# Kernel tuning notes

Measured on AMD Instinct MI355X. Metric: run time of the kernel, lower is better.

Reference implementation:

```python
import jax, jax.numpy as jnp
import numpy as np

EPS = 1e-15


def setup_inputs() -> dict:
    key = jax.random.key(0)
    k1, k2, k3 = jax.random.split(key, 3)
    B, F, C, T = 8, 257, 8, 3000
    X_real = jax.random.normal(k1, (B, F, C, T), dtype=jnp.float32)
    X_imag = jax.random.normal(k2, (B, F, C, T), dtype=jnp.float32)
    mask = jax.random.uniform(k3, (B, F, T), dtype=jnp.float32)
    return {"X_real": X_real, "X_imag": X_imag, "mask": mask}


def reference(X_real, X_imag, mask):
    # X: (B, F, C, T) complex STFT
    X = X_real + 1j * X_imag
    # normalize mask over time (normalize=True)
    m = mask / (jnp.sum(mask, axis=-1, keepdims=True) + EPS)  # (B,F,T)
    # Fused masked time-weighted outer product: equivalent to
    # einsum('...ct,...et->...tce') * mask then sum over t, but contracts
    # t directly (batched GEMM) without the (B,F,T,C,C) intermediate.
    Xm = X * m[..., None, :]                                  # (B,F,C,T)
    psd = jnp.einsum('bfct,bfet->bfce', Xm, jnp.conj(X))      # (B,F,C,C)
    return psd
```

## Files before the change

kernel.cpp:

```cpp
#include <hip/hip_runtime.h>

#define T_LEN 3000
#define TQ2 1500
#define C_CH 8
#define NTHREADS 256
#define NWAVES 4


#define XPOSE_ROUND(OFF)                                        \
    {                                                           \
        const bool hi = (lane & (OFF)) != 0;                    \
        _Pragma("unroll")                                       \
        for (int i = 0; i < (OFF); ++i) {                       \
            float send = hi ? acc[i] : acc[i + (OFF)];          \
            float recv = __shfl_xor(send, (OFF));               \
            float keep = hi ? acc[i + (OFF)] : acc[i];          \
            acc[i] = keep + recv;                               \
        }                                                       \
    }

__global__ __launch_bounds__(NTHREADS) void psd_kernel(
        const float* __restrict__ Xr,
        const float* __restrict__ Xi,
        const float* __restrict__ Mk,
        float* __restrict__ out,
        int real_elems, int write_imag) {
    const int slice = blockIdx.x;
    const int tid   = threadIdx.x;
    const int lane  = tid & 63;
    const int wave  = tid >> 6;

    const float2* xr2 = reinterpret_cast<const float2*>(Xr) + (size_t)slice * (C_CH * TQ2);
    const float2* xi2 = reinterpret_cast<const float2*>(Xi) + (size_t)slice * (C_CH * TQ2);
    const float2* mk2 = reinterpret_cast<const float2*>(Mk) + (size_t)slice * TQ2;

    float acc[64];
#pragma unroll
    for (int k = 0; k < 64; ++k) acc[k] = 0.f;
    float s = 0.f;

    for (int q = tid; q < TQ2; q += NTHREADS) {
        float2 mv = mk2[q];
        s += mv.x + mv.y;
        float ar[C_CH][2], ai[C_CH][2];
#pragma unroll
        for (int c = 0; c < C_CH; ++c) {
            float2 v = xr2[c * TQ2 + q];
            ar[c][0] = v.x; ar[c][1] = v.y;
            float2 w = xi2[c * TQ2 + q];
            ai[c][0] = w.x; ai[c][1] = w.y;
        }
        const float mm[2] = {mv.x, mv.y};
#pragma unroll
        for (int j = 0; j < 2; ++j) {
            const float m = mm[j];
            float mr[C_CH], mi[C_CH];
#pragma unroll
            for (int c = 0; c < C_CH; ++c) {
                mr[c] = m * ar[c][j];
                mi[c] = m * ai[c][j];
            }
#pragma unroll
            for (int c = 0; c < C_CH; ++c)
                acc[c] += mr[c] * ar[c][j] + mi[c] * ai[c][j];
#pragma unroll
            for (int c = 0; c < C_CH; ++c) {
#pragma unroll
                for (int e = c + 1; e < C_CH; ++e) {
                    const int p = 7 * c - (c * (c - 1)) / 2 + (e - c - 1);
                    acc[8 + p]  += mr[c] * ar[e][j] + mi[c] * ai[e][j];
                    acc[36 + p] += mi[c] * ar[e][j] - mr[c] * ai[e][j];
                }
            }
        }
    }

#pragma unroll
    for (int off = 32; off > 0; off >>= 1) s += __shfl_xor(s, off);

    XPOSE_ROUND(32)
    XPOSE_ROUND(16)
    XPOSE_ROUND(8)
    XPOSE_ROUND(4)
    XPOSE_ROUND(2)
    XPOSE_ROUND(1)

    __shared__ float red[NWAVES * 64];
    __shared__ float sred[NWAVES];
    __shared__ float fin[128];
    red[wave * 64 + lane] = acc[0];
    if (lane == 0) sred[wave] = s;
    __syncthreads();

    if (tid < 64) {
        float tot = (red[tid] + red[64 + tid]) + (red[128 + tid] + red[192 + tid]);
        const float stot = (sred[0] + sred[1]) + (sred[2] + sred[3]);
        tot *= 1.0f / (stot + 1e-15f);

        if (tid < 8) {
            const int c = tid;
            fin[c * 8 + c]      = tot;
            fin[64 + c * 8 + c] = 0.f;
        } else {
            int p = (tid < 36) ? (tid - 8) : (tid - 36);
            int c = 0;
            while (p >= 7 - c) { p -= 7 - c; ++c; }
            const int e = c + 1 + p;
            if (tid < 36) {
                fin[c * 8 + e] = tot;
                fin[e * 8 + c] = tot;
            } else {
                fin[64 + c * 8 + e] = tot;
                fin[64 + e * 8 + c] = -tot;
            }
        }
    }
    __syncthreads();
    if (tid < 64) {
        out[(size_t)slice * 64 + tid] = fin[tid];
    } else if (tid < 128 && write_imag) {
        out[(size_t)real_elems + (size_t)slice * 64 + (tid - 64)] = fin[tid];
    }
}

extern "C" void kernel_launch(void* const* d_in, const int* in_sizes, int n_in,
                              void* d_out, int out_size, void* d_ws, size_t ws_size,
                              hipStream_t stream) {
    const float* Xr = (const float*)d_in[0];
    const float* Xi = (const float*)d_in[1];
    const float* Mk = (const float*)d_in[2];
    float* out = (float*)d_out;
    const int slices = in_sizes[2] / T_LEN;
    const int real_elems = slices * 64;
    const int write_imag = (out_size >= 2 * real_elems) ? 1 : 0;
    psd_kernel<<<dim3(slices), dim3(NTHREADS), 0, stream>>>(Xr, Xi, Mk, out,
                                                            real_elems, write_imag);
}
```

Measured before the change: 404.1 us.

## Double-buffer time chunks into LDS with async global_load_lds prefetch

New measurement: 410.6 us. About the same (+1.6%).

```diff
diff --git a/kernel.cpp b/kernel.cpp
--- a/kernel.cpp
+++ b/kernel.cpp
@@ -1,11 +1,17 @@
 #include <hip/hip_runtime.h>
 
 #define T_LEN 3000
-#define TQ2 1500
 #define C_CH 8
 #define NTHREADS 256
 #define NWAVES 4
+#define TT 256
+#define NCHUNK 12
+#define NSTREAM 17
 
+#define AS1 __attribute__((address_space(1)))
+#define AS3 __attribute__((address_space(3)))
+#define GLOAD_LDS(G, L) \
+    __builtin_amdgcn_global_load_lds((const AS1 void*)(G), (AS3 void*)(L), 16, 0, 0)
 
 #define XPOSE_ROUND(OFF)                                        \
     {                                                           \
@@ -19,7 +25,29 @@
         }                                                       \
     }
 
-__global__ __launch_bounds__(NTHREADS) void psd_kernel(
+__device__ __forceinline__ void stage(const float* __restrict__ Xr,
+                                      const float* __restrict__ Xi,
+                                      const float* __restrict__ Mk,
+                                      float* buf, int slice, int off,
+                                      int wave, int lane) {
+    int elem = off + lane * 4;
+    if (elem > T_LEN - 4) elem = T_LEN - 4;
+    const size_t xbase = (size_t)slice * (C_CH * T_LEN);
+#pragma unroll
+    for (int k = 0; k < 4; ++k) {
+        const int s = wave + 4 * k;
+        const float* g = (s < 8)
+            ? (Xr + xbase + (size_t)s * T_LEN + elem)
+            : (Xi + xbase + (size_t)(s - 8) * T_LEN + elem);
+        GLOAD_LDS(g, buf + s * TT);
+    }
+    if (wave == 0) {
+        const float* g = Mk + (size_t)slice * T_LEN + elem;
+        GLOAD_LDS(g, buf + 16 * TT);
+    }
+}
+
+__global__ __launch_bounds__(NTHREADS, 4) void psd_kernel(
         const float* __restrict__ Xr,
         const float* __restrict__ Xi,
         const float* __restrict__ Mk,
@@ -30,49 +58,62 @@
     const int lane  = tid & 63;
     const int wave  = tid >> 6;
 
-    const float2* xr2 = reinterpret_cast<const float2*>(Xr) + (size_t)slice * (C_CH * TQ2);
-    const float2* xi2 = reinterpret_cast<const float2*>(Xi) + (size_t)slice * (C_CH * TQ2);
-    const float2* mk2 = reinterpret_cast<const float2*>(Mk) + (size_t)slice * TQ2;
+    __shared__ float lds[2][NSTREAM * TT];
+    __shared__ float red[NWAVES * 64];
+    __shared__ float sred[NWAVES];
+    __shared__ float fin[128];
 
     float acc[64];
 #pragma unroll
     for (int k = 0; k < 64; ++k) acc[k] = 0.f;
     float s = 0.f;
 
-    for (int q = tid; q < TQ2; q += NTHREADS) {
-        float2 mv = mk2[q];
-        s += mv.x + mv.y;
-        float ar[C_CH][2], ai[C_CH][2];
+    stage(Xr, Xi, Mk, lds[0], slice, 0, wave, lane);
+
+    for (int ch = 0; ch < NCHUNK; ++ch) {
+        const int cur = ch & 1;
+        if (ch + 1 < NCHUNK) {
+            stage(Xr, Xi, Mk, lds[cur ^ 1], slice, (ch + 1) * TT, wave, lane);
+            if (wave == 0) asm volatile("s_waitcnt vmcnt(5)" ::: "memory");
+            else           asm volatile("s_waitcnt vmcnt(4)" ::: "memory");
+        } else {
+            asm volatile("s_waitcnt vmcnt(0)" ::: "memory");
+        }
+        __builtin_amdgcn_s_barrier();
+
+        const int rem   = T_LEN - ch * TT;
+        const int valid = rem < TT ? rem : TT;
+        const float* buf = lds[cur];
+        if (tid < valid) {
+            const float m = buf[16 * TT + tid];
+            s += m;
+            float xr[C_CH], xi[C_CH];
 #pragma unroll
-        for (int c = 0; c < C_CH; ++c) {
-            float2 v = xr2[c * TQ2 + q];
-            ar[c][0] = v.x; ar[c][1] = v.y;
-            float2 w = xi2[c * TQ2 + q];
-            ai[c][0] = w.x; ai[c][1] = w.y;
-        }
-        const float mm[2] = {mv.x, mv.y};
-#pragma unroll
-        for (int j = 0; j < 2; ++j) {
-            const float m = mm[j];
+            for (int c = 0; c < C_CH; ++c) {
+                xr[c] = buf[c * TT + tid];
+                xi[c] = buf[(8 + c) * TT + tid];
+            }
             float mr[C_CH], mi[C_CH];
 #pragma unroll
             for (int c = 0; c < C_CH; ++c) {
-                mr[c] = m * ar[c][j];
-                mi[c] = m * ai[c][j];
+                mr[c] = m * xr[c];
+                mi[c] = m * xi[c];
             }
 #pragma unroll
             for (int c = 0; c < C_CH; ++c)
-                acc[c] += mr[c] * ar[c][j] + mi[c] * ai[c][j];
+                acc[c] += mr[c] * xr[c] + mi[c] * xi[c];
 #pragma unroll
             for (int c = 0; c < C_CH; ++c) {
 #pragma unroll
                 for (int e = c + 1; e < C_CH; ++e) {
                     const int p = 7 * c - (c * (c - 1)) / 2 + (e - c - 1);
-                    acc[8 + p]  += mr[c] * ar[e][j] + mi[c] * ai[e][j];
-                    acc[36 + p] += mi[c] * ar[e][j] - mr[c] * ai[e][j];
+                    acc[8 + p]  += mr[c] * xr[e] + mi[c] * xi[e];
+                    acc[36 + p] += mi[c] * xr[e] - mr[c] * xi[e];
                 }
             }
         }
+        asm volatile("" ::: "memory");
+        __builtin_amdgcn_s_barrier();
     }
 
 #pragma unroll
@@ -85,9 +126,6 @@
     XPOSE_ROUND(2)
     XPOSE_ROUND(1)
 
-    __shared__ float red[NWAVES * 64];
-    __shared__ float sred[NWAVES];
-    __shared__ float fin[128];
     red[wave * 64 + lane] = acc[0];
     if (lane == 0) sred[wave] = s;
     __syncthreads();
```
